# Performance work log

Hardware: AMD Instinct MI355X
Metric: run time of the kernel (lower is better)

The kernel has to match this reference:

```python
import jax, jax.numpy as jnp
import numpy as np

ALPHA = 1.0


def setup_inputs() -> dict:
    key = jax.random.key(0)
    k1, k2 = jax.random.split(key)
    N, K, D = 200000, 256, 256
    z = jax.random.normal(k1, (N, D), dtype=jnp.float32)
    # xavier_normal_ for a [K, D] parameter: std = sqrt(2 / (K + D))
    std = np.sqrt(2.0 / (K + D)).astype(np.float32)
    cluster_centers = jax.random.normal(k2, (K, D), dtype=jnp.float32) * std
    return {"z": z, "cluster_centers": cluster_centers}


def reference(z, cluster_centers):
    # Pairwise squared distances via GEMM expansion: ||z||^2 + ||c||^2 - 2 z.c^T
    # Same math as sum((z[:,None,:] - c[None,:,:])**2, axis=2), without the
    # O(N*K*D) broadcasted intermediate.
    z_sq = jnp.sum(z * z, axis=1, keepdims=True)            # [N, 1]
    c_sq = jnp.sum(cluster_centers * cluster_centers, axis=1)  # [K]
    cross = z @ cluster_centers.T                            # [N, K]
    dist = z_sq + c_sq[None, :] - 2.0 * cross                # [N, K]
    dist = jnp.maximum(dist, 0.0)  # numerical clamp (exact form is >= 0)
    q = 1.0 / (1.0 + dist / ALPHA)
    q = q ** ((ALPHA + 1.0) / 2.0)
    q = q / jnp.sum(q, axis=1, keepdims=True)                # row normalize
    return q
```

## Files before the change

### kernel.cpp

```cpp
#include <hip/hip_runtime.h>
#include <hip/hip_bf16.h>
#include <stdint.h>
#include <stddef.h>


#define NT 512
#define GRID 256
#define PAIRS (GRID * 4)
#define D 256
#define KC 256

typedef __attribute__((ext_vector_type(8))) short short8;
typedef __attribute__((ext_vector_type(4))) float f32x4;

__device__ __forceinline__ short f2bf(float f) {
    uint32_t u = __builtin_bit_cast(uint32_t, f);
    u += 0x7FFFu + ((u >> 16) & 1u);
    return (short)(u >> 16);
}

__device__ __forceinline__ unsigned int pk2(float a, float b) {
    __hip_bfloat162 h = __float22bfloat162_rn(make_float2(a, b));
    unsigned int r;
    __builtin_memcpy(&r, &h, 4);
    return r;
}

__global__ void prep_csq(const float* __restrict__ C, float* __restrict__ csq) {
    const int k = blockIdx.x;
    const int l = threadIdx.x;
    float4 v = *(const float4*)(C + k * D + l * 4);
    float s = v.x * v.x + v.y * v.y + v.z * v.z + v.w * v.w;
#pragma unroll
    for (int off = 32; off > 0; off >>= 1) s += __shfl_down(s, off);
    if (l == 0) csq[k] = s;
}

__global__ void prep_reorder(const float* __restrict__ C, unsigned short* __restrict__ Bf) {
    const int kk = blockIdx.x >> 4;
    const int ct = blockIdx.x & 15;
    const int lane = threadIdx.x;
    const int l15 = lane & 15;
    const int lg = lane >> 4;
    const float* src = C + (size_t)(ct * 16 + l15) * D + kk * 32 + lg * 8;
    float4 a0 = *(const float4*)(src);
    float4 a1 = *(const float4*)(src + 4);
    ushort4 p0, p1;
    p0.x = (unsigned short)f2bf(a0.x); p0.y = (unsigned short)f2bf(a0.y);
    p0.z = (unsigned short)f2bf(a0.z); p0.w = (unsigned short)f2bf(a0.w);
    p1.x = (unsigned short)f2bf(a1.x); p1.y = (unsigned short)f2bf(a1.y);
    p1.z = (unsigned short)f2bf(a1.z); p1.w = (unsigned short)f2bf(a1.w);
    unsigned short* dst = Bf + ((size_t)(kk * 16 + ct) * 64 + lane) * 8;
    *(ushort4*)(dst) = p0;
    *(ushort4*)(dst + 4) = p1;
}

__global__ void __launch_bounds__(NT)
main_kernel(const float* __restrict__ z,
            const uint4* __restrict__ Bf,
            const float* __restrict__ csq,
            float* __restrict__ out, int ntiles) {
    __shared__ uint4 ldsB[8192];
    __shared__ __align__(16) float ldsRS[2][8][16];

    const int tid  = threadIdx.x;
    const int lane = tid & 63;
    const int wave = tid >> 6;
    const int l15  = lane & 15;
    const int lg   = lane >> 4;
    const int half = wave & 1;
    const int pair = wave >> 1;

#pragma unroll
    for (int i = 0; i < 16; ++i) ldsB[tid + i * NT] = Bf[tid + i * NT];
    __syncthreads();

    float csqr[8];
#pragma unroll
    for (int ct = 0; ct < 8; ++ct) csqr[ct] = csq[half * 128 + ct * 16 + l15];

    const char* ldsb = (const char*)ldsB;
    const int laneoff = (lane << 4) + (half << 13);

    const int niter = (ntiles - blockIdx.x * 4 + PAIRS - 1) / PAIRS;

    int t = blockIdx.x * 4 + pair;

    const float* zrow = z + (size_t)(t * 16 + l15) * D + lg * 8;
    float4 S0[4], S1[4];
#pragma unroll
    for (int s = 0; s < 4; ++s) {
        S0[s] = *(const float4*)(zrow + s * 32);
        S1[s] = *(const float4*)(zrow + s * 32 + 4);
    }

    for (int i = 0; i < niter; ++i) {
        const bool active = t < ntiles;
        const int tn = t + PAIRS;
        const int tnc = (tn < ntiles) ? tn : (ntiles - 1);
        const float* zrow_n = z + (size_t)(tnc * 16 + l15) * D + lg * 8;

        f32x4 acc[8];
        const f32x4 zero4 = {0.f, 0.f, 0.f, 0.f};
#pragma unroll
        for (int ct = 0; ct < 8; ++ct) acc[ct] = zero4;
        float zsq_part = 0.f;

#pragma unroll
        for (int kk = 0; kk < 8; ++kk) {
            float4 c0 = S0[kk & 3], c1 = S1[kk & 3];
            const float* pf = (kk < 4) ? (zrow + (kk + 4) * 32) : (zrow_n + (kk - 4) * 32);
            S0[kk & 3] = *(const float4*)(pf);
            S1[kk & 3] = *(const float4*)(pf + 4);

            zsq_part += c0.x * c0.x + c0.y * c0.y + c0.z * c0.z + c0.w * c0.w +
                        c1.x * c1.x + c1.y * c1.y + c1.z * c1.z + c1.w * c1.w;
            uint4 u;
            u.x = pk2(c0.x, c0.y); u.y = pk2(c0.z, c0.w);
            u.z = pk2(c1.x, c1.y); u.w = pk2(c1.z, c1.w);
            short8 af;
            __builtin_memcpy(&af, &u, 16);
#pragma unroll
            for (int ct = 0; ct < 8; ++ct) {
                short8 bf = *(const short8*)(ldsb + laneoff + ((kk * 16 + ct) << 10));
                acc[ct] = __builtin_amdgcn_mfma_f32_16x16x32_bf16(af, bf, acc[ct], 0, 0, 0);
            }
        }

        float zsq = zsq_part;
        zsq += __shfl_xor(zsq, 16);
        zsq += __shfl_xor(zsq, 32);
        float zsqj[4];
#pragma unroll
        for (int j = 0; j < 4; ++j) zsqj[j] = __shfl(zsq, lg * 4 + j);

        float rs[4] = {0.f, 0.f, 0.f, 0.f};
#pragma unroll
        for (int ct = 0; ct < 8; ++ct) {
#pragma unroll
            for (int j = 0; j < 4; ++j) {
                float dist = zsqj[j] + csqr[ct] - 2.0f * acc[ct][j];
                dist = fmaxf(dist, 0.f);
                float qv = 1.0f / (1.0f + dist);
                acc[ct][j] = qv;
                rs[j] += qv;
            }
        }
#pragma unroll
        for (int j = 0; j < 4; ++j) {
            float s = rs[j];
            s += __shfl_xor(s, 1);
            s += __shfl_xor(s, 2);
            s += __shfl_xor(s, 4);
            s += __shfl_xor(s, 8);
            rs[j] = s;
        }
        if (l15 == 0) {
            float4 w = {rs[0], rs[1], rs[2], rs[3]};
            *(float4*)&ldsRS[i & 1][wave][lg * 4] = w;
        }
        asm volatile("s_waitcnt lgkmcnt(0)" ::: "memory");
        __builtin_amdgcn_s_barrier();
        __builtin_amdgcn_sched_barrier(0);
        float4 prs = *(const float4*)&ldsRS[i & 1][wave ^ 1][lg * 4];
        float inv[4];
        inv[0] = 1.0f / (rs[0] + prs.x);
        inv[1] = 1.0f / (rs[1] + prs.y);
        inv[2] = 1.0f / (rs[2] + prs.z);
        inv[3] = 1.0f / (rs[3] + prs.w);

        if (active) {
#pragma unroll
            for (int j = 0; j < 4; ++j) {
                float* orow = out + (size_t)(t * 16 + lg * 4 + j) * KC + half * 128 + l15;
#pragma unroll
                for (int ct = 0; ct < 8; ++ct) orow[ct * 16] = acc[ct][j] * inv[j];
            }
        }
        t = tn;
        zrow = zrow_n;
    }
}

extern "C" void kernel_launch(void* const* d_in, const int* in_sizes, int n_in,
                              void* d_out, int out_size, void* d_ws, size_t ws_size,
                              hipStream_t stream) {
    const float* zp = (const float*)d_in[0];
    const float* Cp = (const float*)d_in[1];
    const int N = in_sizes[0] / D;
    unsigned short* Bf = (unsigned short*)d_ws;
    float* csq = (float*)((char*)d_ws + (size_t)KC * D * sizeof(unsigned short));

    prep_csq<<<KC, 64, 0, stream>>>(Cp, csq);
    prep_reorder<<<128, 64, 0, stream>>>(Cp, Bf);

    const int ntiles = (N + 15) / 16;
    main_kernel<<<GRID, NT, 0, stream>>>(zp, (const uint4*)Bf, csq, (float*)d_out, ntiles);
}
```

Baseline: 101.6 us.

## Process two 16-row tiles per wave to reuse LDS B fragments

Each wave now handles a 32-row unit (two 16-row tiles) per iteration, so every B fragment read from LDS feeds two MFMAs instead of one. The aim is to halve LDS reads per MFMA and to amortise the per-iteration barrier and reductions over twice the work. The prefetch depth per tile drops from 4 to 2 k-slices, and register pressure roughly doubles for accumulators. The tile count is halved with ntiles>>1, so an odd leftover tile would be dropped; this does not occur at N=200000.

```diff
diff --git a/kernel.cpp b/kernel.cpp
--- a/kernel.cpp
+++ b/kernel.cpp
@@ -6,7 +6,7 @@
 
 #define NT 512
 #define GRID 256
-#define PAIRS (GRID * 4)
+#define UNITS (GRID * 4)
 #define D 256
 #define KC 256
 
@@ -61,7 +61,7 @@
             const float* __restrict__ csq,
             float* __restrict__ out, int ntiles) {
     __shared__ uint4 ldsB[8192];
-    __shared__ __align__(16) float ldsRS[2][8][16];
+    __shared__ __align__(16) float ldsRS[2][8][2][16];
 
     const int tid  = threadIdx.x;
     const int lane = tid & 63;
@@ -82,103 +82,136 @@
     const char* ldsb = (const char*)ldsB;
     const int laneoff = (lane << 4) + (half << 13);
 
-    const int niter = (ntiles - blockIdx.x * 4 + PAIRS - 1) / PAIRS;
-
-    int t = blockIdx.x * 4 + pair;
-
-    const float* zrow = z + (size_t)(t * 16 + l15) * D + lg * 8;
-    float4 S0[4], S1[4];
-#pragma unroll
-    for (int s = 0; s < 4; ++s) {
-        S0[s] = *(const float4*)(zrow + s * 32);
-        S1[s] = *(const float4*)(zrow + s * 32 + 4);
+    const int nunits = ntiles >> 1;
+    const int niter = (nunits - blockIdx.x * 4 + UNITS - 1) / UNITS;
+
+    int u = blockIdx.x * 4 + pair;
+
+    const float* zrow_a = z + ((size_t)u * 32 + l15) * D + lg * 8;
+    const float* zrow_b = zrow_a + 16 * D;
+    float4 Sa0[2], Sa1[2], Sb0[2], Sb1[2];
+#pragma unroll
+    for (int s = 0; s < 2; ++s) {
+        Sa0[s] = *(const float4*)(zrow_a + s * 32);
+        Sa1[s] = *(const float4*)(zrow_a + s * 32 + 4);
+        Sb0[s] = *(const float4*)(zrow_b + s * 32);
+        Sb1[s] = *(const float4*)(zrow_b + s * 32 + 4);
     }
 
     for (int i = 0; i < niter; ++i) {
-        const bool active = t < ntiles;
-        const int tn = t + PAIRS;
-        const int tnc = (tn < ntiles) ? tn : (ntiles - 1);
-        const float* zrow_n = z + (size_t)(tnc * 16 + l15) * D + lg * 8;
-
-        f32x4 acc[8];
+        const bool active = u < nunits;
+        const int un = u + UNITS;
+        const int unc = (un < nunits) ? un : (nunits - 1);
+        const float* zrow_na = z + ((size_t)unc * 32 + l15) * D + lg * 8;
+        const float* zrow_nb = zrow_na + 16 * D;
+
+        f32x4 accA[8], accB[8];
         const f32x4 zero4 = {0.f, 0.f, 0.f, 0.f};
 #pragma unroll
-        for (int ct = 0; ct < 8; ++ct) acc[ct] = zero4;
-        float zsq_part = 0.f;
+        for (int ct = 0; ct < 8; ++ct) { accA[ct] = zero4; accB[ct] = zero4; }
+        float zsq_a = 0.f, zsq_b = 0.f;
 
 #pragma unroll
         for (int kk = 0; kk < 8; ++kk) {
-            float4 c0 = S0[kk & 3], c1 = S1[kk & 3];
-            const float* pf = (kk < 4) ? (zrow + (kk + 4) * 32) : (zrow_n + (kk - 4) * 32);
-            S0[kk & 3] = *(const float4*)(pf);
-            S1[kk & 3] = *(const float4*)(pf + 4);
-
-            zsq_part += c0.x * c0.x + c0.y * c0.y + c0.z * c0.z + c0.w * c0.w +
-                        c1.x * c1.x + c1.y * c1.y + c1.z * c1.z + c1.w * c1.w;
-            uint4 u;
-            u.x = pk2(c0.x, c0.y); u.y = pk2(c0.z, c0.w);
-            u.z = pk2(c1.x, c1.y); u.w = pk2(c1.z, c1.w);
-            short8 af;
-            __builtin_memcpy(&af, &u, 16);
+            float4 ca0 = Sa0[kk & 1], ca1 = Sa1[kk & 1];
+            float4 cb0 = Sb0[kk & 1], cb1 = Sb1[kk & 1];
+            const float* pfa = (kk < 6) ? (zrow_a + (kk + 2) * 32) : (zrow_na + (kk - 6) * 32);
+            const float* pfb = (kk < 6) ? (zrow_b + (kk + 2) * 32) : (zrow_nb + (kk - 6) * 32);
+            Sa0[kk & 1] = *(const float4*)(pfa);
+            Sa1[kk & 1] = *(const float4*)(pfa + 4);
+            Sb0[kk & 1] = *(const float4*)(pfb);
+            Sb1[kk & 1] = *(const float4*)(pfb + 4);
+
+            zsq_a += ca0.x * ca0.x + ca0.y * ca0.y + ca0.z * ca0.z + ca0.w * ca0.w +
+                     ca1.x * ca1.x + ca1.y * ca1.y + ca1.z * ca1.z + ca1.w * ca1.w;
+            zsq_b += cb0.x * cb0.x + cb0.y * cb0.y + cb0.z * cb0.z + cb0.w * cb0.w +
+                     cb1.x * cb1.x + cb1.y * cb1.y + cb1.z * cb1.z + cb1.w * cb1.w;
+            uint4 ua, ub;
+            ua.x = pk2(ca0.x, ca0.y); ua.y = pk2(ca0.z, ca0.w);
+            ua.z = pk2(ca1.x, ca1.y); ua.w = pk2(ca1.z, ca1.w);
+            ub.x = pk2(cb0.x, cb0.y); ub.y = pk2(cb0.z, cb0.w);
+            ub.z = pk2(cb1.x, cb1.y); ub.w = pk2(cb1.z, cb1.w);
+            short8 afa, afb;
+            __builtin_memcpy(&afa, &ua, 16);
+            __builtin_memcpy(&afb, &ub, 16);
 #pragma unroll
             for (int ct = 0; ct < 8; ++ct) {
                 short8 bf = *(const short8*)(ldsb + laneoff + ((kk * 16 + ct) << 10));
-                acc[ct] = __builtin_amdgcn_mfma_f32_16x16x32_bf16(af, bf, acc[ct], 0, 0, 0);
-            }
-        }
-
-        float zsq = zsq_part;
-        zsq += __shfl_xor(zsq, 16);
-        zsq += __shfl_xor(zsq, 32);
-        float zsqj[4];
-#pragma unroll
-        for (int j = 0; j < 4; ++j) zsqj[j] = __shfl(zsq, lg * 4 + j);
-
-        float rs[4] = {0.f, 0.f, 0.f, 0.f};
+                accA[ct] = __builtin_amdgcn_mfma_f32_16x16x32_bf16(afa, bf, accA[ct], 0, 0, 0);
+                accB[ct] = __builtin_amdgcn_mfma_f32_16x16x32_bf16(afb, bf, accB[ct], 0, 0, 0);
+            }
+        }
+
+        float zsqj_a[4], zsqj_b[4];
+        {
+            float za = zsq_a;
+            za += __shfl_xor(za, 16);
+            za += __shfl_xor(za, 32);
+            float zb = zsq_b;
+            zb += __shfl_xor(zb, 16);
+            zb += __shfl_xor(zb, 32);
+#pragma unroll
+            for (int j = 0; j < 4; ++j) {
+                zsqj_a[j] = __shfl(za, lg * 4 + j);
+                zsqj_b[j] = __shfl(zb, lg * 4 + j);
+            }
+        }
+
+        float rsA[4] = {0.f, 0.f, 0.f, 0.f}, rsB[4] = {0.f, 0.f, 0.f, 0.f};
 #pragma unroll
         for (int ct = 0; ct < 8; ++ct) {
 #pragma unroll
             for (int j = 0; j < 4; ++j) {
-                float dist = zsqj[j] + csqr[ct] - 2.0f * acc[ct][j];
-                dist = fmaxf(dist, 0.f);
-                float qv = 1.0f / (1.0f + dist);
-                acc[ct][j] = qv;
-                rs[j] += qv;
+                float da = zsqj_a[j] + csqr[ct] - 2.0f * accA[ct][j];
+                float db = zsqj_b[j] + csqr[ct] - 2.0f * accB[ct][j];
+                da = fmaxf(da, 0.f);
+                db = fmaxf(db, 0.f);
+                float qa = 1.0f / (1.0f + da);
+                float qb = 1.0f / (1.0f + db);
+                accA[ct][j] = qa; rsA[j] += qa;
+                accB[ct][j] = qb; rsB[j] += qb;
             }
         }
 #pragma unroll
         for (int j = 0; j < 4; ++j) {
-            float s = rs[j];
-            s += __shfl_xor(s, 1);
-            s += __shfl_xor(s, 2);
-            s += __shfl_xor(s, 4);
-            s += __shfl_xor(s, 8);
-            rs[j] = s;
+            float sa = rsA[j], sb = rsB[j];
+            sa += __shfl_xor(sa, 1); sb += __shfl_xor(sb, 1);
+            sa += __shfl_xor(sa, 2); sb += __shfl_xor(sb, 2);
+            sa += __shfl_xor(sa, 4); sb += __shfl_xor(sb, 4);
+            sa += __shfl_xor(sa, 8); sb += __shfl_xor(sb, 8);
+            rsA[j] = sa; rsB[j] = sb;
         }
         if (l15 == 0) {
-            float4 w = {rs[0], rs[1], rs[2], rs[3]};
-            *(float4*)&ldsRS[i & 1][wave][lg * 4] = w;
+            float4 wa = {rsA[0], rsA[1], rsA[2], rsA[3]};
+            float4 wb = {rsB[0], rsB[1], rsB[2], rsB[3]};
+            *(float4*)&ldsRS[i & 1][wave][0][lg * 4] = wa;
+            *(float4*)&ldsRS[i & 1][wave][1][lg * 4] = wb;
         }
         asm volatile("s_waitcnt lgkmcnt(0)" ::: "memory");
         __builtin_amdgcn_s_barrier();
         __builtin_amdgcn_sched_barrier(0);
-        float4 prs = *(const float4*)&ldsRS[i & 1][wave ^ 1][lg * 4];
-        float inv[4];
-        inv[0] = 1.0f / (rs[0] + prs.x);
-        inv[1] = 1.0f / (rs[1] + prs.y);
-        inv[2] = 1.0f / (rs[2] + prs.z);
-        inv[3] = 1.0f / (rs[3] + prs.w);
+        float4 pa = *(const float4*)&ldsRS[i & 1][wave ^ 1][0][lg * 4];
+        float4 pb = *(const float4*)&ldsRS[i & 1][wave ^ 1][1][lg * 4];
+        float invA[4], invB[4];
+        invA[0] = 1.0f / (rsA[0] + pa.x); invB[0] = 1.0f / (rsB[0] + pb.x);
+        invA[1] = 1.0f / (rsA[1] + pa.y); invB[1] = 1.0f / (rsB[1] + pb.y);
+        invA[2] = 1.0f / (rsA[2] + pa.z); invB[2] = 1.0f / (rsB[2] + pb.z);
+        invA[3] = 1.0f / (rsA[3] + pa.w); invB[3] = 1.0f / (rsB[3] + pb.w);
 
         if (active) {
 #pragma unroll
             for (int j = 0; j < 4; ++j) {
-                float* orow = out + (size_t)(t * 16 + lg * 4 + j) * KC + half * 128 + l15;
-#pragma unroll
-                for (int ct = 0; ct < 8; ++ct) orow[ct * 16] = acc[ct][j] * inv[j];
-            }
-        }
-        t = tn;
-        zrow = zrow_n;
+                float* orow = out + ((size_t)u * 32 + lg * 4 + j) * KC + half * 128 + l15;
+#pragma unroll
+                for (int ct = 0; ct < 8; ++ct) {
+                    orow[ct * 16] = accA[ct][j] * invA[j];
+                    orow[16 * KC + ct * 16] = accB[ct][j] * invB[j];
+                }
+            }
+        }
+        u = un;
+        zrow_a = zrow_na;
+        zrow_b = zrow_nb;
     }
 }
 
```

New measurement: 120.9 us. +19.0%, slower.
